# Kernel tuning notes

Measured on AMD Instinct MI355X. Metric: run time of the kernel, lower is better.

## Reference

```python
import jax, jax.numpy as jnp
import numpy as np

B, S, D, VOCAB = 8, 32, 256, 50257
N = 4 * 64          # n_devices * neurons_per_device
K = max(N // 5, 8)  # top-k active neurons = 51


def _make_edges():
    # mimics the torch init loop: 4*N random (src,dst) draws, keep src!=dst, dedup, preserve order
    rng = np.random.default_rng(0)
    s = rng.integers(0, N, 4 * N)
    d = rng.integers(0, N, 4 * N)
    seen, es, ed = set(), [], []
    for a, b in zip(s.tolist(), d.tolist()):
        if a != b and (a, b) not in seen:
            seen.add((a, b)); es.append(a); ed.append(b)
    return np.asarray(es, np.int32), np.asarray(ed, np.int32)


def setup_inputs() -> dict:
    key = jax.random.key(0)
    ks = jax.random.split(key, 12)
    es, ed = _make_edges()
    E = es.shape[0]
    f32 = jnp.float32
    return {
        "input_ids": jax.random.randint(ks[0], (B, S), 0, VOCAB),
        "embed":     jax.random.normal(ks[1], (VOCAB, D), f32) * 0.02,
        "pos_embed": jax.random.normal(ks[2], (S, D), f32) * 0.02,
        "router_W":  jax.random.normal(ks[3], (N, D), f32) * 0.02,
        "router_b":  jnp.zeros((N,), f32),
        "fc_W":      jax.random.normal(ks[4], (N, D, D), f32) * 0.02,
        "fc_b":      jnp.zeros((N, D), f32),
        "gate_W":    jax.random.normal(ks[5], (N, D), f32) * 0.02,
        "gate_b":    jnp.zeros((N,), f32),
        "conn_W":    jax.random.normal(ks[6], (E, D, D), f32) * 0.02,
        "ln_g":      jnp.ones((D,), f32),
        "ln_b":      jnp.zeros((D,), f32),
        "out_W":     jax.random.normal(ks[7], (VOCAB, D), f32) * 0.02,
        "out_b":     jnp.zeros((VOCAB,), f32),
        "edge_src":  jnp.asarray(es),
        "edge_dst":  jnp.asarray(ed),
    }


def _forward(input_ids, embed, pos_embed, router_W, router_b, fc_W, fc_b,
             gate_W, gate_b, conn_W, ln_g, ln_b, out_W, out_b, edge_src, edge_dst):
    x = embed[input_ids] + pos_embed[None, :, :]  # [B,S,D]

    def propagate(xt):  # xt: [B,D] -> [B,D]
        scores = xt @ router_W.T + router_b                  # [B,N]
        vals, idx = jax.lax.top_k(scores, K)                 # [B,K]
        active = idx[0]                                      # batch-elem-0 picks the active set (as in torch code)
        w = jax.nn.softmax(vals, axis=-1)                    # [B,K]
        # hop 0: active neurons applied to routed input
        h = jnp.einsum('bd,kod->kbo', xt, fc_W[active]) + fc_b[active][:, None, :]
        g = jax.nn.sigmoid(jnp.einsum('bd,kd->kb', xt, gate_W[active]) + gate_b[active][:, None])
        states = jax.nn.gelu(h, approximate=False) * g[:, :, None] * w.T[:, :, None]  # [K,B,D]
        # edge pass: only edges with both endpoints active contribute
        member = jnp.zeros((N,), bool).at[active].set(True)
        pos = jnp.zeros((N,), jnp.int32).at[active].set(jnp.arange(K, dtype=jnp.int32))
        emask = (member[edge_src] & member[edge_dst]).astype(xt.dtype)               # [E]
        sig = jnp.einsum('ebd,eod->ebo', states[pos[edge_src]], conn_W)              # [E,B,D]
        hh = jnp.einsum('ebd,eod->ebo', sig, fc_W[edge_dst]) + fc_b[edge_dst][:, None, :]
        gg = jax.nn.sigmoid(jnp.einsum('ebd,ed->eb', sig, gate_W[edge_dst]) + gate_b[edge_dst][:, None])
        act = jax.nn.gelu(hh, approximate=False) * gg[:, :, None] * emask[:, None, None]
        nxt = jax.ops.segment_sum(act, pos[edge_dst], num_segments=K)                # [K,B,D]
        return (states + 0.5 * nxt).mean(axis=0)                                     # [B,D]

    out = jax.vmap(propagate, in_axes=1, out_axes=1)(x)      # [B,S,D]
    mu = out.mean(-1, keepdims=True)
    var = ((out - mu) ** 2).mean(-1, keepdims=True)
    out = (out - mu) * jax.lax.rsqrt(var + 1e-5) * ln_g + ln_b
    return out @ out_W.T + out_b                             # [B,S,VOCAB]


def reference(input_ids, embed, pos_embed, router_W, router_b, fc_W, fc_b,
              gate_W, gate_b, conn_W, ln_g, ln_b, out_W, out_b, edge_src, edge_dst):
    return _forward(input_ids, embed, pos_embed, router_W, router_b, fc_W, fc_b,
                    gate_W, gate_b, conn_W, ln_g, ln_b, out_W, out_b, edge_src, edge_dst)
```

## Files before the change

### kernel.cpp

```cpp
#include <hip/hip_runtime.h>
#include <math.h>

#define B_ 8
#define S_ 32
#define D_ 256
#define N_ 256
#define K_ 51
#define V_ 50257

__device__ __forceinline__ float dot4f(float4 a, float4 b){
  return a.x*b.x + a.y*b.y + a.z*b.z + a.w*b.w;
}
__device__ __forceinline__ float gelu_exact(float x){
  return 0.5f * x * (1.0f + erff(x * 0.70710678118654752440f));
}
__device__ __forceinline__ float sigmoidf_(float x){
  return 1.0f / (1.0f + expf(-x));
}

__global__ __launch_bounds__(256) void k_embed(const int* __restrict__ ids,
    const float* __restrict__ embed, const float* __restrict__ pose,
    float* __restrict__ xt)
{
  int bx = blockIdx.x;
  int t = bx >> 3, b = bx & 7;
  int d = threadIdx.x;
  int id = ids[b * S_ + t];
  xt[(size_t)bx * D_ + d] = embed[(size_t)id * D_ + d] + pose[(size_t)t * D_ + d];
}

__global__ __launch_bounds__(256) void k_router(const float* __restrict__ xt,
    const float* __restrict__ rW, const float* __restrict__ rb,
    float* __restrict__ scores)
{
  int bx = blockIdx.x;
  int tid = threadIdx.x;
  __shared__ float4 xs4[64];
  if (tid < 64) xs4[tid] = ((const float4*)(xt + (size_t)bx * D_))[tid];
  __syncthreads();
  float acc = rb[tid];
  const float4* wp = (const float4*)(rW + (size_t)tid * D_);
  for (int d4 = 0; d4 < 64; d4++){
    float4 w = wp[d4]; float4 x = xs4[d4];
    acc += dot4f(w, x);
  }
  scores[(size_t)bx * N_ + tid] = acc;
}

__global__ __launch_bounds__(256) void k_topk(const float* __restrict__ scores,
    float* __restrict__ wbuf, int* __restrict__ active,
    int* __restrict__ member, int* __restrict__ pos)
{
  int bx = blockIdx.x;
  int t = bx >> 3, b = bx & 7;
  int tid = threadIdx.x;
  __shared__ float sv[256];
  __shared__ int   si[256];
  __shared__ float ex[K_];
  __shared__ float exsum;
  sv[tid] = scores[(size_t)bx * N_ + tid];
  si[tid] = tid;
  for (int kk = 2; kk <= 256; kk <<= 1){
    for (int j = kk >> 1; j > 0; j >>= 1){
      __syncthreads();
      int ixj = tid ^ j;
      if (ixj > tid){
        float va = sv[tid], vb = sv[ixj];
        int   ia = si[tid], ib = si[ixj];
        bool before = (va > vb) || (va == vb && ia < ib);
        bool up = ((tid & kk) == 0);
        if (up != before){
          sv[tid] = vb; sv[ixj] = va;
          si[tid] = ib; si[ixj] = ia;
        }
      }
    }
  }
  __syncthreads();
  float vmax = sv[0];
  if (tid < K_) ex[tid] = expf(sv[tid] - vmax);
  __syncthreads();
  if (tid == 0){
    float s = 0.0f;
    for (int k = 0; k < K_; k++) s += ex[k];
    exsum = s;
  }
  __syncthreads();
  if (tid < K_) wbuf[(size_t)bx * K_ + tid] = ex[tid] / exsum;
  if (b == 0){
    member[t * N_ + tid] = 0;
    pos[t * N_ + tid] = 0;
    __syncthreads();
    if (tid < K_){
      int nn = si[tid];
      active[t * K_ + tid] = nn;
      member[t * N_ + nn] = 1;
      pos[t * N_ + nn] = tid;
    }
  }
}

__global__ __launch_bounds__(256) void k_compact(const int* __restrict__ esrc,
    const int* __restrict__ edst, const int* __restrict__ member,
    int E, int* __restrict__ count, unsigned int* __restrict__ items)
{
  int idx = blockIdx.x * 256 + threadIdx.x;
  if (idx >= E * S_) return;
  int e = idx % E, t = idx / E;
  int src = esrc[e], dst = edst[e];
  if (member[t * N_ + src] && member[t * N_ + dst]){
    int slot = atomicAdd(count, 1);
    items[slot] = ((unsigned int)t << 16) | (unsigned int)e;
  }
}

__global__ __launch_bounds__(256) void k_hop0(const float* __restrict__ xt,
    const float* __restrict__ fcW, const float* __restrict__ fcB,
    const float* __restrict__ gateW, const float* __restrict__ gateB,
    const float* __restrict__ wbuf, const int* __restrict__ active,
    float* __restrict__ states)
{
  int k = blockIdx.x, t = blockIdx.y;
  int tid = threadIdx.x;
  __shared__ float xs[B_ * D_];
  __shared__ float gl[B_];
  __shared__ float wl[B_];
  int n = active[t * K_ + k];
  float4* xs4 = (float4*)xs;
  const float4* xt4 = (const float4*)(xt + (size_t)t * B_ * D_);
  #pragma unroll
  for (int i = 0; i < 2; i++) xs4[tid + i * 256] = xt4[tid + i * 256];
  if (tid < B_) wl[tid] = wbuf[(size_t)(t * B_ + tid) * K_ + k];
  __syncthreads();
  {
    int wave = tid >> 6, lane = tid & 63;
    float4 gw = ((const float4*)(gateW + (size_t)n * D_))[lane];
    float a0 = dot4f(gw, xs4[(wave * 2 + 0) * 64 + lane]);
    float a1 = dot4f(gw, xs4[(wave * 2 + 1) * 64 + lane]);
    for (int s2 = 1; s2 < 64; s2 <<= 1){
      a0 += __shfl_xor(a0, s2, 64);
      a1 += __shfl_xor(a1, s2, 64);
    }
    if (lane == 0){
      float gb = gateB[n];
      gl[wave * 2 + 0] = sigmoidf_(a0 + gb);
      gl[wave * 2 + 1] = sigmoidf_(a1 + gb);
    }
  }
  __syncthreads();
  float acc[B_] = {0,0,0,0,0,0,0,0};
  const float4* wp = (const float4*)(fcW + (size_t)n * D_ * D_ + (size_t)tid * D_);
  for (int d4 = 0; d4 < 64; d4++){
    float4 w = wp[d4];
    #pragma unroll
    for (int b = 0; b < B_; b++) acc[b] += dot4f(w, xs4[b * 64 + d4]);
  }
  float fb = fcB[(size_t)n * D_ + tid];
  #pragma unroll
  for (int b = 0; b < B_; b++){
    float s = gelu_exact(acc[b] + fb) * gl[b] * wl[b];
    states[((size_t)(t * K_ + k) * B_ + b) * D_ + tid] = s;
  }
}

__global__ __launch_bounds__(256) void k_edge2(const float* __restrict__ states,
    const float* __restrict__ connW, const float* __restrict__ fcW,
    const float* __restrict__ fcB, const float* __restrict__ gateW,
    const float* __restrict__ gateB, const int* __restrict__ esrc,
    const int* __restrict__ edst, const int* __restrict__ pos,
    const int* __restrict__ count, const unsigned int* __restrict__ items,
    float* __restrict__ nxt)
{
  __shared__ float xs[B_ * D_];
  __shared__ float sg[B_ * D_];
  __shared__ float gl[B_];
  int n_items = *count;
  int tid = threadIdx.x;
  float4* xs4 = (float4*)xs;
  float4* sg4 = (float4*)sg;
  for (int it = blockIdx.x; it < n_items; it += gridDim.x){
    unsigned int pk = items[it];
    int t = (int)(pk >> 16), e = (int)(pk & 0xFFFFu);
    int src = esrc[e], dst = edst[e];
    int ks = pos[t * N_ + src], kd = pos[t * N_ + dst];
    const float4* st4 = (const float4*)(states + (size_t)(t * K_ + ks) * B_ * D_);
    #pragma unroll
    for (int i = 0; i < 2; i++) xs4[tid + i * 256] = st4[tid + i * 256];
    __syncthreads();
    {
      float acc[B_] = {0,0,0,0,0,0,0,0};
      const float4* wp = (const float4*)(connW + (size_t)e * D_ * D_ + (size_t)tid * D_);
      for (int d4 = 0; d4 < 64; d4++){
        float4 w = wp[d4];
        #pragma unroll
        for (int b = 0; b < B_; b++) acc[b] += dot4f(w, xs4[b * 64 + d4]);
      }
      #pragma unroll
      for (int b = 0; b < B_; b++) sg[b * D_ + tid] = acc[b];
    }
    __syncthreads();
    {
      int wave = tid >> 6, lane = tid & 63;
      float4 gw = ((const float4*)(gateW + (size_t)dst * D_))[lane];
      float a0 = dot4f(gw, sg4[(wave * 2 + 0) * 64 + lane]);
      float a1 = dot4f(gw, sg4[(wave * 2 + 1) * 64 + lane]);
      for (int s2 = 1; s2 < 64; s2 <<= 1){
        a0 += __shfl_xor(a0, s2, 64);
        a1 += __shfl_xor(a1, s2, 64);
      }
      if (lane == 0){
        float gb = gateB[dst];
        gl[wave * 2 + 0] = sigmoidf_(a0 + gb);
        gl[wave * 2 + 1] = sigmoidf_(a1 + gb);
      }
    }
    __syncthreads();
    {
      float acc[B_] = {0,0,0,0,0,0,0,0};
      const float4* wp = (const float4*)(fcW + (size_t)dst * D_ * D_ + (size_t)tid * D_);
      for (int d4 = 0; d4 < 64; d4++){
        float4 w = wp[d4];
        #pragma unroll
        for (int b = 0; b < B_; b++) acc[b] += dot4f(w, sg4[b * 64 + d4]);
      }
      float fb = fcB[(size_t)dst * D_ + tid];
      float* nx = nxt + (size_t)(t * K_ + kd) * B_ * D_;
      #pragma unroll
      for (int b = 0; b < B_; b++){
        float a = gelu_exact(acc[b] + fb) * gl[b];
        atomicAdd(&nx[b * D_ + tid], a);
      }
    }
    __syncthreads();
  }
}

__global__ __launch_bounds__(256) void k_ln(const float* __restrict__ states,
    const float* __restrict__ nxt, const float* __restrict__ lng,
    const float* __restrict__ lnb, float* __restrict__ normed)
{
  int row = blockIdx.x;
  int b = row >> 5, t = row & 31;
  int d = threadIdx.x;
  float v = 0.0f;
  for (int k = 0; k < K_; k++){
    size_t idx = ((size_t)(t * K_ + k) * B_ + b) * D_ + d;
    v += states[idx] + 0.5f * nxt[idx];
  }
  v /= 51.0f;
  __shared__ float red[256];
  red[d] = v; __syncthreads();
  for (int s = 128; s > 0; s >>= 1){ if (d < s) red[d] += red[d + s]; __syncthreads(); }
  float mu = red[0] * (1.0f / 256.0f);
  __syncthreads();
  float c = v - mu;
  red[d] = c * c; __syncthreads();
  for (int s = 128; s > 0; s >>= 1){ if (d < s) red[d] += red[d + s]; __syncthreads(); }
  float var = red[0] * (1.0f / 256.0f);
  normed[(size_t)row * D_ + d] = c * rsqrtf(var + 1e-5f) * lng[d] + lnb[d];
}

__global__ __launch_bounds__(256) void k_logits(const float* __restrict__ normed,
    const float* __restrict__ outW, const float* __restrict__ outB,
    float* __restrict__ out)
{
  __shared__ float Ws[64][132];
  __shared__ float Xs[64][68];
  int tid = threadIdx.x;
  int vbase = blockIdx.x * 128;
  int rbase = blockIdx.y * 64;
  int cg = tid & 31;
  int rg = tid >> 5;
  float acc[8][4];
  #pragma unroll
  for (int i = 0; i < 8; i++)
    #pragma unroll
    for (int j = 0; j < 4; j++) acc[i][j] = 0.0f;

  for (int kb = 0; kb < 4; kb++){
    if (kb) __syncthreads();
    #pragma unroll
    for (int i = 0; i < 8; i++){
      int idx = tid + i * 256;
      int v = idx >> 4, kq = idx & 15;
      int gv = vbase + v;
      float4 w = make_float4(0.0f, 0.0f, 0.0f, 0.0f);
      if (gv < V_) w = ((const float4*)(outW + (size_t)gv * D_))[kb * 16 + kq];
      Ws[kq * 4 + 0][v] = w.x;
      Ws[kq * 4 + 1][v] = w.y;
      Ws[kq * 4 + 2][v] = w.z;
      Ws[kq * 4 + 3][v] = w.w;
    }
    #pragma unroll
    for (int i = 0; i < 4; i++){
      int idx = tid + i * 256;
      int r = idx >> 4, kq = idx & 15;
      float4 x = ((const float4*)(normed + (size_t)(rbase + r) * D_))[kb * 16 + kq];
      Xs[kq * 4 + 0][r] = x.x;
      Xs[kq * 4 + 1][r] = x.y;
      Xs[kq * 4 + 2][r] = x.z;
      Xs[kq * 4 + 3][r] = x.w;
    }
    __syncthreads();
    #pragma unroll 4
    for (int k = 0; k < 64; k++){
      float4 wv = *(const float4*)&Ws[k][cg * 4];
      float4 x0 = *(const float4*)&Xs[k][rg * 8];
      float4 x1 = *(const float4*)&Xs[k][rg * 8 + 4];
      float xr[8] = {x0.x, x0.y, x0.z, x0.w, x1.x, x1.y, x1.z, x1.w};
      float wc[4] = {wv.x, wv.y, wv.z, wv.w};
      #pragma unroll
      for (int i = 0; i < 8; i++)
        #pragma unroll
        for (int j = 0; j < 4; j++)
          acc[i][j] = fmaf(xr[i], wc[j], acc[i][j]);
    }
  }
  #pragma unroll
  for (int j = 0; j < 4; j++){
    int gc = vbase + cg * 4 + j;
    if (gc < V_){
      float ob = outB[gc];
      #pragma unroll
      for (int i = 0; i < 8; i++)
        out[(size_t)(rbase + rg * 8 + i) * V_ + gc] = acc[i][j] + ob;
    }
  }
}

extern "C" void kernel_launch(void* const* d_in, const int* in_sizes, int n_in,
                              void* d_out, int out_size, void* d_ws, size_t ws_size,
                              hipStream_t stream)
{
  const int*   ids    = (const int*)d_in[0];
  const float* embed  = (const float*)d_in[1];
  const float* pose   = (const float*)d_in[2];
  const float* rW     = (const float*)d_in[3];
  const float* rb     = (const float*)d_in[4];
  const float* fcW    = (const float*)d_in[5];
  const float* fcB    = (const float*)d_in[6];
  const float* gateW  = (const float*)d_in[7];
  const float* gateB  = (const float*)d_in[8];
  const float* connW  = (const float*)d_in[9];
  const float* lng    = (const float*)d_in[10];
  const float* lnb    = (const float*)d_in[11];
  const float* outW   = (const float*)d_in[12];
  const float* outB   = (const float*)d_in[13];
  const int*   esrc   = (const int*)d_in[14];
  const int*   edst   = (const int*)d_in[15];
  int E = in_sizes[14];
  float* out = (float*)d_out;

  char* ws = (char*)d_ws;
  float* xt     = (float*)(ws + 0);
  float* scores = (float*)(ws + 262144);
  unsigned int* items = (unsigned int*)(ws + 262144);
  float* wbuf   = (float*)(ws + 524288);
  int*   active = (int*)  (ws + 589824);
  int*   count  = (int*)  (ws + 596992);
  int*   member = (int*)  (ws + 598016);
  int*   pos    = (int*)  (ws + 630784);
  float* states = (float*)(ws + 663552);
  float* nxt    = (float*)(ws + 14032896);
  float* normed = (float*)(ws + 27402240);

  hipMemsetAsync(nxt, 0, (size_t)3342336 * 4, stream);

  k_embed  <<<dim3(S_ * B_), 256, 0, stream>>>(ids, embed, pose, xt);
  k_router <<<dim3(S_ * B_), 256, 0, stream>>>(xt, rW, rb, scores);
  k_topk   <<<dim3(S_ * B_), 256, 0, stream>>>(scores, wbuf, active, member, pos);
  hipMemsetAsync(count, 0, 4, stream);
  k_compact<<<dim3((E * S_ + 255) / 256), 256, 0, stream>>>(esrc, edst, member, E, count, items);
  k_hop0   <<<dim3(K_, S_), 256, 0, stream>>>(xt, fcW, fcB, gateW, gateB, wbuf, active, states);
  k_edge2  <<<dim3(1280), 256, 0, stream>>>(states, connW, fcW, fcB, gateW, gateB,
                                            esrc, edst, pos, count, items, nxt);
  k_ln     <<<dim3(B_ * S_), 256, 0, stream>>>(states, nxt, lng, lnb, normed);
  k_logits <<<dim3((V_ + 127) / 128, 4), 256, 0, stream>>>(normed, outW, outB, out);
}
```

Baseline: 845.2 us.

## Batch up to two timesteps per edge work item to reuse weight loads

The compaction kernel now walks edges instead of (timestep, edge) pairs. For each edge it builds a bitmask of the timesteps where both endpoints are active and emits chunks that each pair up to two timesteps. The edge kernel processes both timesteps of a chunk together, so each loaded row of conn_W and fc_W feeds two sets of accumulators, halving weight traffic for paired items. The cost is doubled shared memory and register use per block, which may lower occupancy, and the grid size drops from 1280 to 1024 blocks.

```diff
diff --git a/kernel.cpp b/kernel.cpp
--- a/kernel.cpp
+++ b/kernel.cpp
@@ -100,17 +100,22 @@
   }
 }
 
-__global__ __launch_bounds__(256) void k_compact(const int* __restrict__ esrc,
+__global__ __launch_bounds__(256) void k_chunks(const int* __restrict__ esrc,
     const int* __restrict__ edst, const int* __restrict__ member,
-    int E, int* __restrict__ count, unsigned int* __restrict__ items)
-{
-  int idx = blockIdx.x * 256 + threadIdx.x;
-  if (idx >= E * S_) return;
-  int e = idx % E, t = idx / E;
+    int E, int* __restrict__ ccount, unsigned int* __restrict__ chunks)
+{
+  int e = blockIdx.x * 256 + threadIdx.x;
+  if (e >= E) return;
   int src = esrc[e], dst = edst[e];
-  if (member[t * N_ + src] && member[t * N_ + dst]){
-    int slot = atomicAdd(count, 1);
-    items[slot] = ((unsigned int)t << 16) | (unsigned int)e;
+  unsigned int mask = 0;
+  for (int t = 0; t < S_; t++)
+    if (member[t * N_ + src] && member[t * N_ + dst]) mask |= (1u << t);
+  while (mask){
+    int t0 = __ffs(mask) - 1; mask &= mask - 1;
+    unsigned int t1 = 0xFFu;
+    if (mask){ t1 = (unsigned int)(__ffs(mask) - 1); mask &= mask - 1; }
+    int ci = atomicAdd(ccount, 1);
+    chunks[ci] = (unsigned int)e | ((unsigned int)t0 << 16) | (t1 << 24);
   }
 }
 
@@ -163,72 +168,117 @@
   }
 }
 
-__global__ __launch_bounds__(256) void k_edge2(const float* __restrict__ states,
+__global__ __launch_bounds__(256) void k_edge3(const float* __restrict__ states,
     const float* __restrict__ connW, const float* __restrict__ fcW,
     const float* __restrict__ fcB, const float* __restrict__ gateW,
     const float* __restrict__ gateB, const int* __restrict__ esrc,
     const int* __restrict__ edst, const int* __restrict__ pos,
-    const int* __restrict__ count, const unsigned int* __restrict__ items,
+    const int* __restrict__ ccount, const unsigned int* __restrict__ chunks,
     float* __restrict__ nxt)
 {
-  __shared__ float xs[B_ * D_];
-  __shared__ float sg[B_ * D_];
-  __shared__ float gl[B_];
-  int n_items = *count;
+  __shared__ float xs[2 * B_ * D_];
+  __shared__ float sg[2 * B_ * D_];
+  __shared__ float gl[16];
+  int nch = *ccount;
   int tid = threadIdx.x;
   float4* xs4 = (float4*)xs;
   float4* sg4 = (float4*)sg;
-  for (int it = blockIdx.x; it < n_items; it += gridDim.x){
-    unsigned int pk = items[it];
-    int t = (int)(pk >> 16), e = (int)(pk & 0xFFFFu);
+  for (int it = blockIdx.x; it < nch; it += gridDim.x){
+    unsigned int pk = chunks[it];
+    int e  = (int)(pk & 0xFFFFu);
+    int t0 = (int)((pk >> 16) & 0xFFu);
+    int t1 = (int)((pk >> 24) & 0xFFu);
+    int nc = (t1 == 0xFF) ? 1 : 2;
     int src = esrc[e], dst = edst[e];
-    int ks = pos[t * N_ + src], kd = pos[t * N_ + dst];
-    const float4* st4 = (const float4*)(states + (size_t)(t * K_ + ks) * B_ * D_);
-    #pragma unroll
-    for (int i = 0; i < 2; i++) xs4[tid + i * 256] = st4[tid + i * 256];
-    __syncthreads();
+    int ks0 = pos[t0 * N_ + src], kd0 = pos[t0 * N_ + dst];
     {
-      float acc[B_] = {0,0,0,0,0,0,0,0};
+      const float4* s0 = (const float4*)(states + (size_t)(t0 * K_ + ks0) * B_ * D_);
+      xs4[tid] = s0[tid]; xs4[tid + 256] = s0[tid + 256];
+      if (nc == 2){
+        int ks1 = pos[t1 * N_ + src];
+        const float4* s1 = (const float4*)(states + (size_t)(t1 * K_ + ks1) * B_ * D_);
+        xs4[tid + 512] = s1[tid]; xs4[tid + 768] = s1[tid + 256];
+      }
+    }
+    __syncthreads();
+    {
       const float4* wp = (const float4*)(connW + (size_t)e * D_ * D_ + (size_t)tid * D_);
-      for (int d4 = 0; d4 < 64; d4++){
-        float4 w = wp[d4];
+      if (nc == 2){
+        float a0[B_] = {0,0,0,0,0,0,0,0};
+        float a1[B_] = {0,0,0,0,0,0,0,0};
+        #pragma unroll 16
+        for (int d4 = 0; d4 < 64; d4++){
+          float4 w = wp[d4];
+          #pragma unroll
+          for (int b = 0; b < B_; b++){
+            a0[b] += dot4f(w, xs4[b * 64 + d4]);
+            a1[b] += dot4f(w, xs4[512 + b * 64 + d4]);
+          }
+        }
         #pragma unroll
-        for (int b = 0; b < B_; b++) acc[b] += dot4f(w, xs4[b * 64 + d4]);
+        for (int b = 0; b < B_; b++){
+          sg[b * D_ + tid] = a0[b];
+          sg[2048 + b * D_ + tid] = a1[b];
+        }
+      } else {
+        float a0[B_] = {0,0,0,0,0,0,0,0};
+        #pragma unroll 16
+        for (int d4 = 0; d4 < 64; d4++){
+          float4 w = wp[d4];
+          #pragma unroll
+          for (int b = 0; b < B_; b++) a0[b] += dot4f(w, xs4[b * 64 + d4]);
+        }
+        #pragma unroll
+        for (int b = 0; b < B_; b++) sg[b * D_ + tid] = a0[b];
       }
-      #pragma unroll
-      for (int b = 0; b < B_; b++) sg[b * D_ + tid] = acc[b];
     }
     __syncthreads();
     {
-      int wave = tid >> 6, lane = tid & 63;
-      float4 gw = ((const float4*)(gateW + (size_t)dst * D_))[lane];
-      float a0 = dot4f(gw, sg4[(wave * 2 + 0) * 64 + lane]);
-      float a1 = dot4f(gw, sg4[(wave * 2 + 1) * 64 + lane]);
-      for (int s2 = 1; s2 < 64; s2 <<= 1){
-        a0 += __shfl_xor(a0, s2, 64);
-        a1 += __shfl_xor(a1, s2, 64);
+      int wv = tid >> 6, ln = tid & 63;
+      float4 gw = ((const float4*)(gateW + (size_t)dst * D_))[ln];
+      float gb = gateB[dst];
+      for (int p = wv; p < 8 * nc; p += 4){
+        float a = dot4f(gw, sg4[(p >> 3) * 512 + (p & 7) * 64 + ln]);
+        for (int s2 = 1; s2 < 64; s2 <<= 1) a += __shfl_xor(a, s2, 64);
+        if (ln == 0) gl[p] = sigmoidf_(a + gb);
       }
-      if (lane == 0){
-        float gb = gateB[dst];
-        gl[wave * 2 + 0] = sigmoidf_(a0 + gb);
-        gl[wave * 2 + 1] = sigmoidf_(a1 + gb);
-      }
     }
     __syncthreads();
     {
-      float acc[B_] = {0,0,0,0,0,0,0,0};
-      const float4* wp = (const float4*)(fcW + (size_t)dst * D_ * D_ + (size_t)tid * D_);
-      for (int d4 = 0; d4 < 64; d4++){
-        float4 w = wp[d4];
+      const float4* wq = (const float4*)(fcW + (size_t)dst * D_ * D_ + (size_t)tid * D_);
+      float fb = fcB[(size_t)dst * D_ + tid];
+      if (nc == 2){
+        float b0[B_] = {0,0,0,0,0,0,0,0};
+        float b1[B_] = {0,0,0,0,0,0,0,0};
+        #pragma unroll 16
+        for (int d4 = 0; d4 < 64; d4++){
+          float4 w = wq[d4];
+          #pragma unroll
+          for (int b = 0; b < B_; b++){
+            b0[b] += dot4f(w, sg4[b * 64 + d4]);
+            b1[b] += dot4f(w, sg4[512 + b * 64 + d4]);
+          }
+        }
+        int kd1 = pos[t1 * N_ + dst];
+        float* nx0 = nxt + (size_t)(t0 * K_ + kd0) * B_ * D_;
+        float* nx1 = nxt + (size_t)(t1 * K_ + kd1) * B_ * D_;
         #pragma unroll
-        for (int b = 0; b < B_; b++) acc[b] += dot4f(w, sg4[b * 64 + d4]);
-      }
-      float fb = fcB[(size_t)dst * D_ + tid];
-      float* nx = nxt + (size_t)(t * K_ + kd) * B_ * D_;
-      #pragma unroll
-      for (int b = 0; b < B_; b++){
-        float a = gelu_exact(acc[b] + fb) * gl[b];
-        atomicAdd(&nx[b * D_ + tid], a);
+        for (int b = 0; b < B_; b++){
+          atomicAdd(&nx0[b * D_ + tid], gelu_exact(b0[b] + fb) * gl[b]);
+          atomicAdd(&nx1[b * D_ + tid], gelu_exact(b1[b] + fb) * gl[8 + b]);
+        }
+      } else {
+        float b0[B_] = {0,0,0,0,0,0,0,0};
+        #pragma unroll 16
+        for (int d4 = 0; d4 < 64; d4++){
+          float4 w = wq[d4];
+          #pragma unroll
+          for (int b = 0; b < B_; b++) b0[b] += dot4f(w, sg4[b * 64 + d4]);
+        }
+        float* nx0 = nxt + (size_t)(t0 * K_ + kd0) * B_ * D_;
+        #pragma unroll
+        for (int b = 0; b < B_; b++)
+          atomicAdd(&nx0[b * D_ + tid], gelu_exact(b0[b] + fb) * gl[b]);
       }
     }
     __syncthreads();
@@ -354,10 +404,10 @@
   char* ws = (char*)d_ws;
   float* xt     = (float*)(ws + 0);
   float* scores = (float*)(ws + 262144);
-  unsigned int* items = (unsigned int*)(ws + 262144);
+  unsigned int* chunks = (unsigned int*)(ws + 262144);
   float* wbuf   = (float*)(ws + 524288);
   int*   active = (int*)  (ws + 589824);
-  int*   count  = (int*)  (ws + 596992);
+  int*   ccount = (int*)  (ws + 596992);
   int*   member = (int*)  (ws + 598016);
   int*   pos    = (int*)  (ws + 630784);
   float* states = (float*)(ws + 663552);
@@ -369,11 +419,11 @@
   k_embed  <<<dim3(S_ * B_), 256, 0, stream>>>(ids, embed, pose, xt);
   k_router <<<dim3(S_ * B_), 256, 0, stream>>>(xt, rW, rb, scores);
   k_topk   <<<dim3(S_ * B_), 256, 0, stream>>>(scores, wbuf, active, member, pos);
-  hipMemsetAsync(count, 0, 4, stream);
-  k_compact<<<dim3((E * S_ + 255) / 256), 256, 0, stream>>>(esrc, edst, member, E, count, items);
+  hipMemsetAsync(ccount, 0, 4, stream);
+  k_chunks <<<dim3((E + 255) / 256), 256, 0, stream>>>(esrc, edst, member, E, ccount, chunks);
   k_hop0   <<<dim3(K_, S_), 256, 0, stream>>>(xt, fcW, fcB, gateW, gateB, wbuf, active, states);
-  k_edge2  <<<dim3(1280), 256, 0, stream>>>(states, connW, fcW, fcB, gateW, gateB,
-                                            esrc, edst, pos, count, items, nxt);
+  k_edge3  <<<dim3(1024), 256, 0, stream>>>(states, connW, fcW, fcB, gateW, gateB,
+                                            esrc, edst, pos, ccount, chunks, nxt);
   k_ln     <<<dim3(B_ * S_), 256, 0, stream>>>(states, nxt, lng, lnb, normed);
   k_logits <<<dim3((V_ + 127) / 128, 4), 256, 0, stream>>>(normed, outW, outB, out);
 }
```

New measurement: 795.8 us. 5.9% less time.
